# Performance work log

Measured on AMD Instinct MI355X. Metric: run time of the kernel, lower is better.

The kernel has to match this reference:

```python
import jax, jax.numpy as jnp
import numpy as np

QSP_DEPTH = 27  # -> 2*depth+1 = 55 phase parameters
B = 524288


def setup_inputs() -> dict:
    key = jax.random.key(0)
    k1, k2, k3 = jax.random.split(key, 3)
    x = jax.random.normal(k1, (B, 1), dtype=jnp.float32)
    qsp_params = jax.random.normal(k2, (2 * QSP_DEPTH + 1,), dtype=jnp.float32)
    alphas = jax.random.normal(k3, (B,), dtype=jnp.float32)
    bias = jnp.zeros((1,), dtype=jnp.float32)
    return {"x": x, "qsp_params": qsp_params, "alphas": alphas, "bias": bias}


def _qsp_expectation(theta, phis):
    """Quantum-signal-processing expectation Re(<0|U|0>) with
    U = S(phi_0) * prod_{k=1}^{2*depth} [ W(theta) S(phi_k) ],
    W(theta) = [[cos t, i sin t], [i sin t, cos t]] (X-rotation signal),
    S(phi) = diag(e^{i phi}, e^{-i phi}) (Z phase rotation).
    theta: (B,) float, phis: (2*depth+1,) float -> (B,) float.
    """
    c = jnp.cos(theta).astype(jnp.complex64)
    s = (1j * jnp.sin(theta).astype(jnp.complex64))
    # W: (B, 2, 2) signal rotation, shared across all chain steps
    W = jnp.stack([jnp.stack([c, s], axis=-1), jnp.stack([s, c], axis=-1)], axis=-2)

    P0 = jnp.broadcast_to(jnp.eye(2, dtype=jnp.complex64), W.shape)

    def step(P, phi):
        e = jnp.exp(1j * phi.astype(jnp.complex64))
        # right-multiply by diag(e, conj(e)) == column scaling of W
        M = W * jnp.stack([e, jnp.conj(e)])[None, None, :]
        return P @ M, None

    P, _ = jax.lax.scan(step, P0, phis[1:])  # 2*depth fixed-depth chain
    # left S(phi_0) only scales row 0 of <0|.|0> element
    amp00 = jnp.exp(1j * phis[0].astype(jnp.complex64)) * P[:, 0, 0]
    return jnp.real(amp00)


def reference(x, qsp_params, alphas, bias):
    theta = x[:, 0]                                   # (B,)
    qsp_val = _qsp_expectation(theta, qsp_params)     # (B,)
    preds = alphas * qsp_val + bias                   # (B,)
    return preds[:, None].astype(jnp.float32)         # (B, 1)
```

## Files before the change

kernel.cpp:

```cpp
#include <hip/hip_runtime.h>
#include <math.h>

constexpr int QSP_DEPTH = 27;
constexpr int NPHI = 2 * QSP_DEPTH + 1;

__global__ __launch_bounds__(256) void qsp_kernel(
    const float* __restrict__ x,
    const float* __restrict__ phis,
    const float* __restrict__ alphas,
    const float* __restrict__ bias,
    float* __restrict__ out,
    int n)
{
    __shared__ float2 tbl[NPHI];
    const int t = threadIdx.x;
    if (t < NPHI) {
        float s, c;
        sincosf(phis[t], &s, &c);
        tbl[t] = make_float2(c, s);
    }
    __syncthreads();

    const int i = blockIdx.x * blockDim.x + t;
    if (i >= n) return;

    const float theta = x[i];
    float st, ct;
    __sincosf(theta, &st, &ct);

    float ur = 1.0f, ui = 0.0f, vr = 0.0f, vi = 0.0f;

#pragma unroll
    for (int k = 1; k < NPHI; ++k) {
        const float ar = ct * ur - st * vi;
        const float ai = ct * ui + st * vr;
        const float br = ct * vr - st * ui;
        const float bi = ct * vi + st * ur;
        const float cp = tbl[k].x, sp = tbl[k].y;
        ur = cp * ar - sp * ai;
        ui = sp * ar + cp * ai;
        vr = cp * br + sp * bi;
        vi = cp * bi - sp * br;
    }

    const float re = tbl[0].x * ur - tbl[0].y * ui;
    out[i] = alphas[i] * re + bias[0];
}

extern "C" void kernel_launch(void* const* d_in, const int* in_sizes, int n_in,
                              void* d_out, int out_size, void* d_ws, size_t ws_size,
                              hipStream_t stream) {
    const float* x      = (const float*)d_in[0];
    const float* phis   = (const float*)d_in[1];
    const float* alphas = (const float*)d_in[2];
    const float* bias   = (const float*)d_in[3];
    float* out          = (float*)d_out;

    const int n = in_sizes[0];
    const int block = 256;
    const int grid = (n + block - 1) / block;
    qsp_kernel<<<grid, block, 0, stream>>>(x, phis, alphas, bias, out, n);
}
```

Before: 75.63 us.

## Precompute QSP Chebyshev coefficients once and evaluate with Clenshaw recurrence

Adds a single-block double-precision kernel that expands the 54-step QSP matrix product into Chebyshev coefficients in cos(2θ), which depend only on the phases. The per-element kernel then runs a 27-term Clenshaw recurrence instead of 54 complex 2x2 updates, so per-thread arithmetic drops sharply. In exchange it adds a second serial tiny kernel launch on the critical path, and float Clenshaw accuracy may differ from the reference chain.

```diff
diff --git a/kernel.cpp b/kernel.cpp
--- a/kernel.cpp
+++ b/kernel.cpp
@@ -2,49 +2,91 @@
 #include <math.h>
 
 constexpr int QSP_DEPTH = 27;
-constexpr int NPHI = 2 * QSP_DEPTH + 1;
+constexpr int NPHI  = 2 * QSP_DEPTH + 1;
+constexpr int NSTEP = NPHI - 1;
+constexpr int MAXM  = NSTEP;
+constexpr int NE    = 2 * MAXM + 1;
+constexpr int NC    = MAXM / 2 + 1;
 
-__global__ __launch_bounds__(256) void qsp_kernel(
+__global__ __launch_bounds__(128) void qsp_coeff_kernel(
+    const float* __restrict__ phis, float* __restrict__ coeffs)
+{
+    __shared__ double Ur[2][NE + 2], Ui[2][NE + 2];
+    __shared__ double Vr[2][NE + 2], Vi[2][NE + 2];
+    __shared__ double cph[NSTEP], sph[NSTEP];
+
+    const int t = threadIdx.x;
+    if (t < NSTEP) {
+        const double p = (double)phis[t + 1];
+        cph[t] = cos(p);
+        sph[t] = sin(p);
+    }
+    if (t < NE + 2) {
+        Ur[0][t] = 0.0; Ui[0][t] = 0.0; Vr[0][t] = 0.0; Vi[0][t] = 0.0;
+        Ur[1][t] = 0.0; Ui[1][t] = 0.0; Vr[1][t] = 0.0; Vi[1][t] = 0.0;
+    }
+    __syncthreads();
+    if (t == 0) Ur[0][MAXM + 1] = 1.0;
+    __syncthreads();
+
+    for (int s = 0; s < NSTEP; ++s) {
+        const int src = s & 1, dst = src ^ 1;
+        if (t < NE) {
+            const int a = t + 1;
+            const double um1r = Ur[src][a - 1], um1i = Ui[src][a - 1];
+            const double up1r = Ur[src][a + 1], up1i = Ui[src][a + 1];
+            const double vm1r = Vr[src][a - 1], vm1i = Vi[src][a - 1];
+            const double vp1r = Vr[src][a + 1], vp1i = Vi[src][a + 1];
+            const double nur = 0.5 * (um1r + up1r + vm1r - vp1r);
+            const double nui = 0.5 * (um1i + up1i + vm1i - vp1i);
+            const double nvr = 0.5 * (um1r - up1r + vm1r + vp1r);
+            const double nvi = 0.5 * (um1i - up1i + vm1i + vp1i);
+            const double c = cph[s], si = sph[s];
+            Ur[dst][a] = c * nur - si * nui;
+            Ui[dst][a] = c * nui + si * nur;
+            Vr[dst][a] = c * nvr + si * nvi;
+            Vi[dst][a] = c * nvi - si * nvr;
+        }
+        __syncthreads();
+    }
+
+    if (t < NC) {
+        const double p0 = (double)phis[0];
+        const double c0 = cos(p0), s0 = sin(p0);
+        const int a = 2 * t + MAXM + 1;
+        const double re = c0 * Ur[0][a] - s0 * Ui[0][a];
+        coeffs[t] = (float)((t ? 2.0 : 1.0) * re);
+    }
+}
+
+__global__ __launch_bounds__(256) void qsp_eval_kernel(
     const float* __restrict__ x,
-    const float* __restrict__ phis,
     const float* __restrict__ alphas,
     const float* __restrict__ bias,
-    float* __restrict__ out,
-    int n)
+    const float* __restrict__ coeffs,
+    float* __restrict__ out, int n)
 {
-    __shared__ float2 tbl[NPHI];
+    __shared__ float cs[NC];
     const int t = threadIdx.x;
-    if (t < NPHI) {
-        float s, c;
-        sincosf(phis[t], &s, &c);
-        tbl[t] = make_float2(c, s);
-    }
+    if (t < NC) cs[t] = coeffs[t];
     __syncthreads();
 
     const int i = blockIdx.x * blockDim.x + t;
     if (i >= n) return;
 
-    const float theta = x[i];
-    float st, ct;
-    __sincosf(theta, &st, &ct);
+    const float th = x[i];
+    const float y  = cosf(2.0f * th);
+    const float y2 = 2.0f * y;
 
-    float ur = 1.0f, ui = 0.0f, vr = 0.0f, vi = 0.0f;
-
+    float b1 = 0.0f, b2 = 0.0f;
 #pragma unroll
-    for (int k = 1; k < NPHI; ++k) {
-        const float ar = ct * ur - st * vi;
-        const float ai = ct * ui + st * vr;
-        const float br = ct * vr - st * ui;
-        const float bi = ct * vi + st * ur;
-        const float cp = tbl[k].x, sp = tbl[k].y;
-        ur = cp * ar - sp * ai;
-        ui = sp * ar + cp * ai;
-        vr = cp * br + sp * bi;
-        vi = cp * bi - sp * br;
+    for (int l = NC - 1; l >= 1; --l) {
+        const float bl = fmaf(y2, b1, cs[l] - b2);
+        b2 = b1;
+        b1 = bl;
     }
-
-    const float re = tbl[0].x * ur - tbl[0].y * ui;
-    out[i] = alphas[i] * re + bias[0];
+    const float res = fmaf(y, b1, cs[0] - b2);
+    out[i] = fmaf(alphas[i], res, bias[0]);
 }
 
 extern "C" void kernel_launch(void* const* d_in, const int* in_sizes, int n_in,
@@ -55,9 +97,13 @@
     const float* alphas = (const float*)d_in[2];
     const float* bias   = (const float*)d_in[3];
     float* out          = (float*)d_out;
+    float* coeffs       = (float*)d_ws;
 
     const int n = in_sizes[0];
+
+    qsp_coeff_kernel<<<1, 128, 0, stream>>>(phis, coeffs);
+
     const int block = 256;
     const int grid = (n + block - 1) / block;
-    qsp_kernel<<<grid, block, 0, stream>>>(x, phis, alphas, bias, out, n);
+    qsp_eval_kernel<<<grid, block, 0, stream>>>(x, alphas, bias, coeffs, out, n);
 }
```

New measurement: 73.88 us. -2.3%, faster.

## Replace per-element QSP chain with Chebyshev polynomial evaluated via Clenshaw

Applied to the files above, without the earlier changes.

Each block first expands the 54-step QSP product symbolically into Chebyshev coefficients in cos(2θ), using a shared-memory ping-pong recurrence. Each element then costs one cosf plus a 27-term Clenshaw recurrence instead of 54 complex 2x2 updates. The kernel also switches to float4 grid-stride loads and stores over a fixed 512-block grid. In exchange, every block redundantly recomputes the coefficients behind 27 barriers, the tail is silently dropped when n is not a multiple of 4, and Clenshaw with many terms may change numerical accuracy.

```diff
diff --git a/kernel.cpp b/kernel.cpp
--- a/kernel.cpp
+++ b/kernel.cpp
@@ -2,49 +2,109 @@
 #include <math.h>
 
 constexpr int QSP_DEPTH = 27;
-constexpr int NPHI = 2 * QSP_DEPTH + 1;
+constexpr int NPHI  = 2 * QSP_DEPTH + 1;
+constexpr int NSTEP = NPHI - 1;
+constexpr int NDBL  = NSTEP / 2;
+constexpr int MAXM  = NSTEP;
+constexpr int NE    = 2 * MAXM + 1;
+constexpr int NA    = NE + 4;
+constexpr int NC    = MAXM / 2 + 1;
+constexpr int NB    = 512;
 
-__global__ __launch_bounds__(256) void qsp_kernel(
+__global__ __launch_bounds__(256) void qsp_fused_kernel(
     const float* __restrict__ x,
     const float* __restrict__ phis,
     const float* __restrict__ alphas,
     const float* __restrict__ bias,
-    float* __restrict__ out,
-    int n)
+    float* __restrict__ out, int n)
 {
-    __shared__ float2 tbl[NPHI];
+    __shared__ float2 U[2][NA], V[2][NA];
+    __shared__ float cph[NSTEP], sph[NSTEP];
+    __shared__ float cs[NC];
+
     const int t = threadIdx.x;
-    if (t < NPHI) {
+
+    if (t < NSTEP) {
         float s, c;
-        sincosf(phis[t], &s, &c);
-        tbl[t] = make_float2(c, s);
+        sincosf(phis[t + 1], &s, &c);
+        cph[t] = c; sph[t] = s;
+    }
+    if (t < NA) {
+        U[0][t] = make_float2(0.f, 0.f); V[0][t] = make_float2(0.f, 0.f);
+        U[1][t] = make_float2(0.f, 0.f); V[1][t] = make_float2(0.f, 0.f);
+    }
+    __syncthreads();
+    if (t == 0) U[0][MAXM + 2] = make_float2(1.f, 0.f);
+    __syncthreads();
+
+    int src = 0;
+    for (int s = 0; s < NDBL; ++s) {
+        const int dst = src ^ 1;
+        if (t < NE) {
+            const int a = t + 2;
+            const float2 um2 = U[src][a - 2], um0 = U[src][a], up2 = U[src][a + 2];
+            const float2 vm2 = V[src][a - 2], vm0 = V[src][a], vp2 = V[src][a + 2];
+            const float ca = cph[2 * s],     sa = sph[2 * s];
+            const float cb = cph[2 * s + 1], sb = sph[2 * s + 1];
+
+            float tr = 0.5f * (um2.x + um0.x + vm2.x - vm0.x);
+            float ti = 0.5f * (um2.y + um0.y + vm2.y - vm0.y);
+            const float uAm1r = ca * tr - sa * ti, uAm1i = ca * ti + sa * tr;
+            tr = 0.5f * (um2.x - um0.x + vm2.x + vm0.x);
+            ti = 0.5f * (um2.y - um0.y + vm2.y + vm0.y);
+            const float vAm1r = ca * tr + sa * ti, vAm1i = ca * ti - sa * tr;
+            tr = 0.5f * (um0.x + up2.x + vm0.x - vp2.x);
+            ti = 0.5f * (um0.y + up2.y + vm0.y - vp2.y);
+            const float uAp1r = ca * tr - sa * ti, uAp1i = ca * ti + sa * tr;
+            tr = 0.5f * (um0.x - up2.x + vm0.x + vp2.x);
+            ti = 0.5f * (um0.y - up2.y + vm0.y + vp2.y);
+            const float vAp1r = ca * tr + sa * ti, vAp1i = ca * ti - sa * tr;
+
+            tr = 0.5f * (uAm1r + uAp1r + vAm1r - vAp1r);
+            ti = 0.5f * (uAm1i + uAp1i + vAm1i - vAp1i);
+            U[dst][a] = make_float2(cb * tr - sb * ti, cb * ti + sb * tr);
+            tr = 0.5f * (uAm1r - uAp1r + vAm1r + vAp1r);
+            ti = 0.5f * (uAm1i - uAp1i + vAm1i + vAp1i);
+            V[dst][a] = make_float2(cb * tr + sb * ti, cb * ti - sb * tr);
+        }
+        src ^= 1;
+        __syncthreads();
+    }
+
+    if (t < NC) {
+        float s0, c0;
+        sincosf(phis[0], &s0, &c0);
+        const float2 u = U[src][2 * t + MAXM + 2];
+        const float re = c0 * u.x - s0 * u.y;
+        cs[t] = (t ? 2.0f : 1.0f) * re;
     }
     __syncthreads();
 
-    const int i = blockIdx.x * blockDim.x + t;
-    if (i >= n) return;
+    const float b0 = bias[0];
+    const int nv = n >> 2;
+    const float4* __restrict__ x4 = (const float4*)x;
+    const float4* __restrict__ a4 = (const float4*)alphas;
+    float4* __restrict__ o4 = (float4*)out;
 
-    const float theta = x[i];
-    float st, ct;
-    __sincosf(theta, &st, &ct);
-
-    float ur = 1.0f, ui = 0.0f, vr = 0.0f, vi = 0.0f;
-
+    for (int i = blockIdx.x * blockDim.x + t; i < nv; i += NB * 256) {
+        const float4 xv = x4[i];
+        const float4 av = a4[i];
+        float4 ov;
+        float* xe = (float*)&xv; float* ae = (float*)&av; float* oe = (float*)&ov;
 #pragma unroll
-    for (int k = 1; k < NPHI; ++k) {
-        const float ar = ct * ur - st * vi;
-        const float ai = ct * ui + st * vr;
-        const float br = ct * vr - st * ui;
-        const float bi = ct * vi + st * ur;
-        const float cp = tbl[k].x, sp = tbl[k].y;
-        ur = cp * ar - sp * ai;
-        ui = sp * ar + cp * ai;
-        vr = cp * br + sp * bi;
-        vi = cp * bi - sp * br;
+        for (int e = 0; e < 4; ++e) {
+            const float y  = cosf(2.0f * xe[e]);
+            const float y2 = 2.0f * y;
+            float b1 = 0.0f, b2 = 0.0f;
+#pragma unroll
+            for (int l = NC - 1; l >= 1; --l) {
+                const float bl = fmaf(y2, b1, cs[l] - b2);
+                b2 = b1; b1 = bl;
+            }
+            oe[e] = fmaf(ae[e], fmaf(y, b1, cs[0] - b2), b0);
+        }
+        o4[i] = ov;
     }
-
-    const float re = tbl[0].x * ur - tbl[0].y * ui;
-    out[i] = alphas[i] * re + bias[0];
 }
 
 extern "C" void kernel_launch(void* const* d_in, const int* in_sizes, int n_in,
@@ -57,7 +117,5 @@
     float* out          = (float*)d_out;
 
     const int n = in_sizes[0];
-    const int block = 256;
-    const int grid = (n + block - 1) / block;
-    qsp_kernel<<<grid, block, 0, stream>>>(x, phis, alphas, bias, out, n);
+    qsp_fused_kernel<<<NB, 256, 0, stream>>>(x, phis, alphas, bias, out, n);
 }
```

Measured after the change: 71.43 us. 1.06x faster.
